# Optimization experiments

Hardware: AMD Instinct MI355X
Metric: run time of the kernel (lower is better)

## Reference

```python
import jax, jax.numpy as jnp
import numpy as np

N_NODES = 100_000
N_EDGES = 1_250_000
N_GRAPHS = 2048


def gcn_conv(x, src, dst, norm, W, b, n):
    # PyG GCNConv: x' = D^-1/2 (A+I) D^-1/2 (x W) + b  (self-loops already in src/dst)
    h = x @ W                                   # [N, 64]
    msg = h[src] * norm[:, None]                # [E+N, 64] gather + scale
    out = jax.ops.segment_sum(msg, dst, num_segments=n)  # scatter-add
    return out + b


def build_norm(edge_index, n):
    # add self loops, compute symmetric gcn normalization
    loop = jnp.arange(n, dtype=edge_index.dtype)
    src = jnp.concatenate([edge_index[0], loop])
    dst = jnp.concatenate([edge_index[1], loop])
    deg = jax.ops.segment_sum(jnp.ones_like(dst, dtype=jnp.float32), dst, num_segments=n)
    dinv = jnp.where(deg > 0, jax.lax.rsqrt(deg), 0.0)
    norm = dinv[src] * dinv[dst]
    return src, dst, norm


def setup_inputs() -> dict:
    key = jax.random.key(0)
    ks = jax.random.split(key, 11)
    return {
        "x": jax.random.randint(ks[0], (N_NODES,), 0, 28, dtype=jnp.int32),
        "edge_index": jax.random.randint(ks[1], (2, N_EDGES), 0, N_NODES, dtype=jnp.int32),
        "edge_attr": jax.random.randint(ks[2], (N_EDGES,), 0, 4, dtype=jnp.int32),
        "batch": jnp.sort(jax.random.randint(ks[3], (N_NODES,), 0, N_GRAPHS, dtype=jnp.int32)),
        "emb_table": jax.random.normal(ks[4], (28, 64), dtype=jnp.float32),
        "W1": jax.random.normal(ks[5], (64, 64), dtype=jnp.float32) * 0.125,
        "b1": jax.random.normal(ks[6], (64,), dtype=jnp.float32) * 0.02,
        "W2": jax.random.normal(ks[7], (64, 64), dtype=jnp.float32) * 0.125,
        "b2": jax.random.normal(ks[8], (64,), dtype=jnp.float32) * 0.02,
        "lin_W": jax.random.normal(ks[9], (64, 1), dtype=jnp.float32) * 0.125,
        "lin_b": jax.random.normal(ks[10], (1,), dtype=jnp.float32) * 0.02,
    }


def reference(x, edge_index, edge_attr, batch, emb_table, W1, b1, W2, b2, lin_W, lin_b):
    n = x.shape[0]
    src, dst, norm = build_norm(edge_index, n)
    h = emb_table[x]                                   # node embedding lookup [N, 64]
    h = jax.nn.relu(gcn_conv(h, src, dst, norm, W1, b1, n))
    # dropout is identity at inference (training=False)
    emb = gcn_conv(h, src, dst, norm, W2, b2, n)        # [N, 64]
    y = emb @ lin_W + lin_b                              # [N, 1]
    out = jax.ops.segment_sum(y, batch, num_segments=N_GRAPHS)  # graph readout
    return out.squeeze(-1)                               # [N_GRAPHS]
```

## Files before the change

kernel.cpp:

```cpp
#include <hip/hip_runtime.h>

#define N_CLS 28
#define DIM   64
#define VB    128
#define VB_SH 7
#define SLK   32
#define NBKT_MAX 1024
#define PT_T  512
#define IPT   12
#define PTILE (PT_T * IPT)

__global__ void __launch_bounds__(PT_T)
k_part(const int* __restrict__ src, const int* __restrict__ dst,
       int* __restrict__ ebkt,
       const float* __restrict__ emb, const float* __restrict__ W1,
       const float* __restrict__ W2, const float* __restrict__ linW,
       const float* __restrict__ b2, const float* __restrict__ linb,
       float* __restrict__ T1g, float* __restrict__ ug, float* __restrict__ ccg,
       float* __restrict__ out,
       int E, int nbkt, int nblk, int out_size) {
    int tid = threadIdx.x, b = blockIdx.x;
    if (b == nblk) {
        int lane = tid & 63, wv = tid >> 6;
        for (int r = wv; r < N_CLS; r += PT_T / 64) {
            float acc = 0.f;
#pragma unroll
            for (int k = 0; k < DIM; ++k) acc += emb[r * DIM + k] * W1[k * DIM + lane];
            T1g[r * DIM + lane] = acc;
        }
        if (wv == 0) {
            float acc = 0.f;
#pragma unroll
            for (int k = 0; k < DIM; ++k) acc += W2[lane * DIM + k] * linW[k];
            ug[lane] = acc;
        }
        if (tid == 0) {
            float s = 0.f;
            for (int k = 0; k < DIM; ++k) s += b2[k] * linW[k];
            ccg[0] = s + linb[0];
        }
        for (int i = tid; i < out_size; i += PT_T) out[i] = 0.f;
        return;
    }
    __shared__ int h[NBKT_MAX];
    for (int i = tid; i < nbkt; i += PT_T) h[i] = 0;
    __syncthreads();
    int s0 = b * PTILE;
    int pk[IPT], ar[IPT];
#pragma unroll
    for (int g = 0; g < IPT / 4; ++g) {
        int i4 = s0 + (g * PT_T + tid) * 4;
        if (i4 + 3 < E) {
            int4 sv = *(const int4*)&src[i4];
            int4 dv = *(const int4*)&dst[i4];
            int ss[4] = {sv.x, sv.y, sv.z, sv.w};
            int dd[4] = {dv.x, dv.y, dv.z, dv.w};
#pragma unroll
            for (int j = 0; j < 4; ++j) {
                int bkt = dd[j] >> VB_SH;
                int r = atomicAdd(&h[bkt], 1);
                pk[g * 4 + j] = ss[j] | ((dd[j] & (VB - 1)) << 17);
                ar[g * 4 + j] = bkt | (r << 10);
            }
        } else {
#pragma unroll
            for (int j = 0; j < 4; ++j) {
                int idx = i4 + j;
                ar[g * 4 + j] = -1;
                if (idx < E) {
                    int s = src[idx], d = dst[idx];
                    int bkt = d >> VB_SH;
                    int r = atomicAdd(&h[bkt], 1);
                    pk[g * 4 + j] = s | ((d & (VB - 1)) << 17);
                    ar[g * 4 + j] = bkt | (r << 10);
                }
            }
        }
    }
    __syncthreads();
    for (int i = tid; i < nbkt; i += PT_T)
        ebkt[((size_t)i * nblk + b) * SLK] = min(h[i], SLK - 1);
#pragma unroll
    for (int k = 0; k < IPT; ++k) {
        int a = ar[k];
        if (a >= 0) {
            int bkt = a & 1023, r = a >> 10;
            if (r < SLK - 1) ebkt[((size_t)bkt * nblk + b) * SLK + 1 + r] = pk[k];
        }
    }
}

#define RUN_FOREACH(rv, BODY)                                            \
    {                                                                    \
        int4 q0 = (rv)[0];                                               \
        int c = q0.x;                                                    \
        int e3[3] = {q0.y, q0.z, q0.w};                                  \
        _Pragma("unroll")                                                \
        for (int j = 0; j < 3; ++j) if (j < c) { int p = e3[j]; BODY; }  \
        for (int base = 3; base < c; base += 4) {                        \
            int4 q = (rv)[(base + 1) >> 2];                              \
            int e4[4] = {q.x, q.y, q.z, q.w};                            \
            _Pragma("unroll")                                            \
            for (int j = 0; j < 4; ++j)                                  \
                if (base + j < c) { int p = e4[j]; BODY; }               \
        }                                                                \
    }

__global__ void __launch_bounds__(256)
k_deg(const int* __restrict__ ebkt, const int* __restrict__ x,
      float2* __restrict__ xd, int N, int nblk) {
    __shared__ int dg[VB];
    int tid = threadIdx.x, k = blockIdx.x;
    if (tid < VB) dg[tid] = 0;
    __syncthreads();
    if (tid < nblk) {
        const int4* rv = (const int4*)(ebkt + ((size_t)k * nblk + tid) * SLK);
        RUN_FOREACH(rv, atomicAdd(&dg[p >> 17], 1));
    }
    __syncthreads();
    int v = k * VB + tid;
    if (tid < VB && v < N)
        xd[v] = make_float2(rsqrtf((float)(dg[tid] + 1)), __int_as_float(x[v]));
}

__global__ void __launch_bounds__(256)
k_l1(const int* __restrict__ ebkt, const float2* __restrict__ xd,
     const float* __restrict__ T1, const float* __restrict__ b1,
     const float* __restrict__ u, float* __restrict__ t, int N, int nblk) {
    __shared__ __align__(16) float cnt[VB * N_CLS];
    __shared__ float T1s[N_CLS * DIM];
    __shared__ float b1s[DIM], us[DIM];
    int tid = threadIdx.x, b = blockIdx.x;
    for (int i = tid; i < VB * N_CLS; i += 256) cnt[i] = 0.f;
    for (int i = tid; i < N_CLS * DIM; i += 256) T1s[i] = T1[i];
    if (tid < DIM) { b1s[tid] = b1[tid]; us[tid] = u[tid]; }
    __syncthreads();
    if (tid < nblk) {
        const int4* rv = (const int4*)(ebkt + ((size_t)b * nblk + tid) * SLK);
        RUN_FOREACH(rv, {
            float2 xs = xd[p & 0x1FFFF];
            atomicAdd(&cnt[(p >> 17) * N_CLS + __float_as_int(xs.y)], xs.x);
        });
    }
    __syncthreads();
    int wave = tid >> 6, lane = tid & 63;
    float tc[N_CLS];
#pragma unroll
    for (int c = 0; c < N_CLS; ++c) tc[c] = T1s[c * DIM + lane];
    int v0 = b * VB;
#pragma unroll 4
    for (int it = 0; it < VB / 4; ++it) {
        int lv = wave * (VB / 4) + it;
        int v = v0 + lv;
        if (v >= N) break;
        float2 pv = xd[v];
        float dv = pv.x;
        int xv = __float_as_int(pv.y);
        const float4* row = (const float4*)&cnt[lv * N_CLS];
        float acc = dv * T1s[xv * DIM + lane];
#pragma unroll
        for (int q4 = 0; q4 < 7; ++q4) {
            float4 r = row[q4];
            acc += r.x * tc[q4 * 4 + 0] + r.y * tc[q4 * 4 + 1]
                 + r.z * tc[q4 * 4 + 2] + r.w * tc[q4 * 4 + 3];
        }
        float hh = fmaxf(dv * acc + b1s[lane], 0.f);
        float q = hh * us[lane];
#pragma unroll
        for (int off = 32; off; off >>= 1) q += __shfl_down(q, off);
        if (lane == 0) t[v] = dv * q;
    }
}

__global__ void __launch_bounds__(256)
k_l2(const int* __restrict__ ebkt, const float2* __restrict__ xd,
     const float* __restrict__ t, const float* __restrict__ cc,
     const int* __restrict__ batch, float* __restrict__ out,
     int N, int n_graphs, int nblk) {
    __shared__ float acc[VB];
    __shared__ float og[64];
    __shared__ int g0s;
    int tid = threadIdx.x, k = blockIdx.x;
    if (tid < VB) acc[tid] = 0.f;
    if (tid < 64) og[tid] = 0.f;
    if (tid == 0) g0s = batch[min(k * VB, N - 1)];
    __syncthreads();
    if (tid < nblk) {
        const int4* rv = (const int4*)(ebkt + ((size_t)k * nblk + tid) * SLK);
        RUN_FOREACH(rv, atomicAdd(&acc[p >> 17], t[p & 0x1FFFF]));
    }
    __syncthreads();
    int v = k * VB + tid;
    if (tid < VB && v < N) {
        float y = xd[v].x * (acc[tid] + t[v]) + cc[0];
        int g = batch[v];
        int off = g - g0s;
        if (off < 64) atomicAdd(&og[off], y);
        else atomicAdd(&out[g], y);
    }
    __syncthreads();
    if (tid < 64) {
        float val = og[tid];
        int g = g0s + tid;
        if (val != 0.f && g < n_graphs) atomicAdd(&out[g], val);
    }
}

extern "C" void kernel_launch(void* const* d_in, const int* in_sizes, int n_in,
                              void* d_out, int out_size, void* d_ws, size_t ws_size,
                              hipStream_t stream) {
    const int*   x     = (const int*)d_in[0];
    const int*   ei    = (const int*)d_in[1];
    const int*   batch = (const int*)d_in[3];
    const float* emb   = (const float*)d_in[4];
    const float* W1    = (const float*)d_in[5];
    const float* b1    = (const float*)d_in[6];
    const float* W2    = (const float*)d_in[7];
    const float* b2    = (const float*)d_in[8];
    const float* linW  = (const float*)d_in[9];
    const float* linb  = (const float*)d_in[10];

    const int N = in_sizes[0];
    const int E = in_sizes[1] / 2;
    const int* srcp = ei;
    const int* dstp = ei + E;
    float* out = (float*)d_out;

    const int nbkt = (N + VB - 1) >> VB_SH;
    const int nblk = (E + PTILE - 1) / PTILE;

    char* w = (char*)d_ws;
    float2* xd   = (float2*)w; w += (size_t)N * 8;
    float*  t    = (float*)w;  w += (size_t)N * 4;
    int*    ebkt = (int*)w;    w += (size_t)nbkt * nblk * SLK * 4;
    float*  T1   = (float*)w;  w += (size_t)N_CLS * DIM * 4;
    float*  u    = (float*)w;  w += DIM * 4;
    float*  cc   = (float*)w;  w += 16;

    k_part<<<nblk + 1, PT_T, 0, stream>>>(srcp, dstp, ebkt,
                                          emb, W1, W2, linW, b2, linb,
                                          T1, u, cc, out, E, nbkt, nblk, out_size);
    k_deg <<<nbkt, 256, 0, stream>>>(ebkt, x, xd, N, nblk);
    k_l1  <<<nbkt, 256, 0, stream>>>(ebkt, xd, T1, b1, u, t, N, nblk);
    k_l2  <<<nbkt, 256, 0, stream>>>(ebkt, xd, t, cc, batch, out, N, out_size, nblk);
}
```

Before: 70.93 us.

## Stage partitioned edges in LDS and write buckets with int4 stores

Bucketed edges are no longer scattered as individual int stores to global memory. Each block first runs a prefix sum over its bucket counts, packs the counts and edges compactly into a shared-memory staging buffer, then copies each bucket out to global with 16-byte vector stores. This is meant to cut uncoalesced scattered global writes, at the cost of extra LDS use, a 1024-wide scan with about ten barriers, and a lower occupancy ceiling. It also hardcodes a bucket limit of 800 in place of 1024, which would overflow if nbkt grew.

Result: no change. 70.55 us (-0.5%).

```diff
diff --git a/kernel.cpp b/kernel.cpp
--- a/kernel.cpp
+++ b/kernel.cpp
@@ -5,10 +5,11 @@
 #define VB    128
 #define VB_SH 7
 #define SLK   32
-#define NBKT_MAX 1024
+#define NBKT_S 800
 #define PT_T  512
 #define IPT   12
 #define PTILE (PT_T * IPT)
+#define STG   9280
 
 __global__ void __launch_bounds__(PT_T)
 k_part(const int* __restrict__ src, const int* __restrict__ dst,
@@ -42,7 +43,10 @@
         for (int i = tid; i < out_size; i += PT_T) out[i] = 0.f;
         return;
     }
-    __shared__ int h[NBKT_MAX];
+    __shared__ int h[NBKT_S];
+    __shared__ int offs[NBKT_S];
+    __shared__ int sc[1024];
+    __shared__ __align__(16) int stage[STG];
     for (int i = tid; i < nbkt; i += PT_T) h[i] = 0;
     __syncthreads();
     int s0 = b * PTILE;
@@ -78,15 +82,36 @@
         }
     }
     __syncthreads();
-    for (int i = tid; i < nbkt; i += PT_T)
-        ebkt[((size_t)i * nblk + b) * SLK] = min(h[i], SLK - 1);
+    int w0 = (tid < nbkt) ? ((min(h[tid], SLK - 1) + 4) & ~3) : 0;
+    int w1 = (tid + 512 < nbkt) ? ((min(h[tid + 512], SLK - 1) + 4) & ~3) : 0;
+    sc[tid] = w0; sc[tid + 512] = w1;
+    __syncthreads();
+    for (int o = 1; o < 1024; o <<= 1) {
+        int a0 = (tid >= o) ? sc[tid - o] : 0;
+        int a1 = (tid + 512 >= o) ? sc[tid + 512 - o] : 0;
+        __syncthreads();
+        sc[tid] += a0; sc[tid + 512] += a1;
+        __syncthreads();
+    }
+    if (tid < nbkt) offs[tid] = sc[tid] - w0;
+    if (tid + 512 < nbkt) offs[tid + 512] = sc[tid + 512] - w1;
+    __syncthreads();
+    for (int i = tid; i < nbkt; i += PT_T) stage[offs[i]] = min(h[i], SLK - 1);
 #pragma unroll
     for (int k = 0; k < IPT; ++k) {
         int a = ar[k];
         if (a >= 0) {
             int bkt = a & 1023, r = a >> 10;
-            if (r < SLK - 1) ebkt[((size_t)bkt * nblk + b) * SLK + 1 + r] = pk[k];
-        }
+            if (r < SLK - 1) stage[offs[bkt] + 1 + r] = pk[k];
+        }
+    }
+    __syncthreads();
+    for (int i = tid; i < nbkt; i += PT_T) {
+        int c = min(h[i], SLK - 1);
+        int nq = (c + 4) >> 2;
+        int4* gq = (int4*)(ebkt + ((size_t)i * nblk + b) * SLK);
+        const int4* sq = (const int4*)&stage[offs[i]];
+        for (int q = 0; q < nq; ++q) gq[q] = sq[q];
     }
 }
 
```
